# Optimization experiments

Measured on AMD Instinct MI355X. Metric: run time of the kernel, lower is better.

## Reference

```python
import jax, jax.numpy as jnp
import numpy as np

C_IN = 128
C_QK = C_IN // 8


def setup_inputs() -> dict:
    key = jax.random.key(0)
    kx, kq, kk, kv = jax.random.split(key, 4)
    x = jax.random.normal(kx, (8, C_IN, 64, 64), dtype=jnp.float32)
    # 1x1 conv weights, stored as (c_out, c_in); fan-in scaled init
    s = 1.0 / np.sqrt(C_IN)
    Wq = jax.random.normal(kq, (C_QK, C_IN), dtype=jnp.float32) * s
    Wk = jax.random.normal(kk, (C_QK, C_IN), dtype=jnp.float32) * s
    Wv = jax.random.normal(kv, (C_IN, C_IN), dtype=jnp.float32) * s
    gamma = jnp.ones((1,), dtype=jnp.float32) * 0.5  # nonzero so residual branch matters
    return {"x": x, "Wq": Wq, "Wk": Wk, "Wv": Wv, "gamma": gamma}


def reference(x, Wq, Wk, Wv, gamma):
    b, c, h, w = x.shape
    xt = rearr = x.reshape(b, c, h * w)            # b c n
    q = jnp.einsum('oc,bcn->bno', Wq, xt)          # b n c//8
    k = jnp.einsum('oc,bcn->bon', Wk, xt)          # b c//8 n
    v = jnp.einsum('oc,bcn->bno', Wv, xt)          # b n c
    energy = jnp.einsum('bno,bom->bnm', q, k)      # b n n (no scale, per source)
    attn = jax.nn.softmax(energy, axis=-1)
    out = jnp.einsum('bnm,bmc->bnc', attn, v)      # b n c
    out = out.transpose(0, 2, 1).reshape(b, c, h, w)
    return x + gamma[0] * out
```

## Files before the change

### kernel.cpp

```cpp
#include <hip/hip_runtime.h>
#include <hip/hip_bf16.h>


typedef __bf16 bf16x8 __attribute__((ext_vector_type(8)));
typedef __bf16 bf16x4 __attribute__((ext_vector_type(4)));
typedef float  f32x16 __attribute__((ext_vector_type(16)));

static constexpr int Bb = 8, Cc = 128, Nn = 4096, CQ = 16;

__device__ __forceinline__ f32x16 mfma32(bf16x8 a, bf16x8 b, f32x16 c) {
    return __builtin_amdgcn_mfma_f32_32x32x16_bf16(a, b, c, 0, 0, 0);
}
struct HL { __bf16 h, l; };
__device__ __forceinline__ HL hilo(float f) {
    HL r;
    r.h = (__bf16)f;
    r.l = (__bf16)(f - (float)r.h);
    return r;
}

__global__ __launch_bounds__(256) void qkv_kernel(
    const float* __restrict__ x, const float* __restrict__ Wq,
    const float* __restrict__ Wk, const float* __restrict__ Wv,
    float* __restrict__ qw, float* __restrict__ kw, __bf16* __restrict__ vw)
{
    const int b = blockIdx.y, n0 = blockIdx.x * 64, t = threadIdx.x;
    const int wave = t >> 6, lane = t & 63, lr = lane & 31, lq = lane >> 5;

    __shared__ __bf16 xh[64][136], xl[64][136];
    __shared__ __bf16 wqh[32][136], wql[32][136];
    __shared__ __bf16 wvh[128][136];

    {
        const int n = t & 63, cib = t >> 6;
        #pragma unroll 4
        for (int i = 0; i < 32; ++i) {
            int ci = cib + i * 4;
            float v = x[((size_t)(b * Cc + ci)) * Nn + n0 + n];
            HL z = hilo(v);
            xh[n][ci] = z.h; xl[n][ci] = z.l;
        }
    }
    #pragma unroll
    for (int i = 0; i < 8; ++i) {
        int idx = t + i * 256;
        int o = idx >> 7, ci = idx & 127;
        HL zq = hilo(Wq[idx]);
        wqh[o][ci] = zq.h; wql[o][ci] = zq.l;
        HL zk = hilo(Wk[idx]);
        wqh[16 + o][ci] = zk.h; wql[16 + o][ci] = zk.l;
    }
    #pragma unroll
    for (int i = 0; i < 16; ++i) {
        int flat = t * 4 + i * 1024;
        float4 w4 = *(const float4*)(Wv + flat);
        int c = flat >> 7, ci0 = flat & 127;
        bf16x4 h4 = { (__bf16)w4.x, (__bf16)w4.y, (__bf16)w4.z, (__bf16)w4.w };
        *(bf16x4*)&wvh[c][ci0] = h4;
    }
    __syncthreads();

    if (wave < 2) {
        const int nh = wave;
        f32x16 acc = {};
        #pragma unroll
        for (int ks = 0; ks < 8; ++ks) {
            bf16x8 ah = *(const bf16x8*)&wqh[lr][ks * 16 + lq * 8];
            bf16x8 al = *(const bf16x8*)&wql[lr][ks * 16 + lq * 8];
            bf16x8 bh = *(const bf16x8*)&xh[nh * 32 + lr][ks * 16 + lq * 8];
            bf16x8 bl = *(const bf16x8*)&xl[nh * 32 + lr][ks * 16 + lq * 8];
            acc = mfma32(ah, bh, acc);
            acc = mfma32(al, bh, acc);
            acc = mfma32(ah, bl, acc);
        }
        const int n = n0 + nh * 32 + lr;
        #pragma unroll
        for (int r = 0; r < 16; ++r) {
            int op = (r & 3) + 8 * (r >> 2) + 4 * lq;
            if (op < 16) qw[((size_t)(b * Nn + n)) * CQ + op] = acc[r];
            else         kw[((size_t)(b * Nn + n)) * CQ + (op - 16)] = acc[r];
        }
    }
    {
        int tl[3][2]; int nt;
        if      (wave == 0) { tl[0][0]=2; tl[0][1]=0; nt=1; }
        else if (wave == 1) { tl[0][0]=2; tl[0][1]=1; nt=1; }
        else if (wave == 2) { tl[0][0]=0; tl[0][1]=0; tl[1][0]=1; tl[1][1]=0; tl[2][0]=3; tl[2][1]=0; nt=3; }
        else                { tl[0][0]=0; tl[0][1]=1; tl[1][0]=1; tl[1][1]=1; tl[2][0]=3; tl[2][1]=1; nt=3; }
        for (int ti = 0; ti < nt; ++ti) {
            const int ct = tl[ti][0], nh = tl[ti][1];
            f32x16 acc = {};
            #pragma unroll
            for (int ks = 0; ks < 8; ++ks) {
                bf16x8 a  = *(const bf16x8*)&wvh[ct * 32 + lr][ks * 16 + lq * 8];
                bf16x8 bh = *(const bf16x8*)&xh[nh * 32 + lr][ks * 16 + lq * 8];
                acc = mfma32(a, bh, acc);
            }
            const int n = n0 + nh * 32 + lr;
            #pragma unroll
            for (int r = 0; r < 16; ++r) {
                int c = (r & 3) + 8 * (r >> 2) + 4 * lq + ct * 32;
                vw[((size_t)(b * Cc + c)) * Nn + n] = (__bf16)acc[r];
            }
        }
    }
}

__global__ __launch_bounds__(256) void attn_kernel(
    const float* __restrict__ x, const float* __restrict__ qw,
    const float* __restrict__ kw, const __bf16* __restrict__ vw,
    const float* __restrict__ gamma, float* __restrict__ out)
{
    const int b = blockIdx.y, n0b = blockIdx.x * 128, t = threadIdx.x;
    const int wave = t >> 6, lane = t & 63, lr = lane & 31, lq = lane >> 5;

    __shared__ __bf16 qT[128][40];
    __shared__ __bf16 kT[64][40];
    __shared__ __bf16 vT[128][72];
    __shared__ __bf16 Pl[4][32][72];

    #pragma unroll
    for (int i = 0; i < 2; ++i) {
        int idx = t + i * 256;
        int n = idx >> 2, og = idx & 3;
        float4 q4 = *(const float4*)(qw + ((size_t)(b * Nn + n0b + n)) * CQ + og * 4);
        HL z0 = hilo(q4.x), z1 = hilo(q4.y), z2 = hilo(q4.z), z3 = hilo(q4.w);
        bf16x4 h = { z0.h, z1.h, z2.h, z3.h };
        bf16x4 l = { z0.l, z1.l, z2.l, z3.l };
        *(bf16x4*)&qT[n][og * 4] = h;
        *(bf16x4*)&qT[n][16 + og * 4] = l;
    }

    const int vc = t >> 3, vs = t & 7;
    const int kr = t >> 2, kg = t & 3;
    uint4 vreg[4]; float4 kreg;

    auto load_chunk = [&](int m0) {
        #pragma unroll
        for (int i = 0; i < 4; ++i)
            vreg[i] = *(const uint4*)(vw + ((size_t)(b * Cc + vc + 32 * i)) * Nn + m0 + vs * 8);
        kreg = *(const float4*)(kw + ((size_t)(b * Nn + m0 + kr)) * CQ + kg * 4);
    };
    auto store_chunk = [&]() {
        #pragma unroll
        for (int i = 0; i < 4; ++i)
            *(uint4*)&vT[vc + 32 * i][vs * 8] = vreg[i];
        HL z0 = hilo(kreg.x), z1 = hilo(kreg.y), z2 = hilo(kreg.z), z3 = hilo(kreg.w);
        bf16x4 h = { z0.h, z1.h, z2.h, z3.h };
        bf16x4 l = { z0.l, z1.l, z2.l, z3.l };
        *(bf16x4*)&kT[kr][kg * 4] = h;
        *(bf16x4*)&kT[kr][16 + kg * 4] = l;
    };

    load_chunk(0);
    store_chunk();
    __syncthreads();

    const bf16x8 qhi = *(const bf16x8*)&qT[wave * 32 + lr][lq * 8];
    const bf16x8 qlo = *(const bf16x8*)&qT[wave * 32 + lr][16 + lq * 8];

    f32x16 acc[4] = {{}, {}, {}, {}};
    float m_run = -3e38f, l_run = 0.f;

    for (int it = 0; it < 64; ++it) {
        load_chunk((it < 63 ? it + 1 : 63) * 64);

        f32x16 s0 = {}, s1 = {};
        {
            bf16x8 kh = *(const bf16x8*)&kT[lr][lq * 8];
            bf16x8 kl = *(const bf16x8*)&kT[lr][16 + lq * 8];
            s0 = mfma32(kh, qhi, s0); s0 = mfma32(kl, qhi, s0); s0 = mfma32(kh, qlo, s0);
            kh = *(const bf16x8*)&kT[32 + lr][lq * 8];
            kl = *(const bf16x8*)&kT[32 + lr][16 + lq * 8];
            s1 = mfma32(kh, qhi, s1); s1 = mfma32(kl, qhi, s1); s1 = mfma32(kh, qlo, s1);
        }

        float cmax = -3e38f;
        #pragma unroll
        for (int r = 0; r < 16; ++r) { cmax = fmaxf(cmax, s0[r]); cmax = fmaxf(cmax, s1[r]); }
        cmax = fmaxf(cmax, __shfl_xor(cmax, 32));
        const float mnew = fmaxf(m_run, cmax);
        const float alpha = __expf(m_run - mnew);
        float p0[16], p1[16], csum = 0.f;
        #pragma unroll
        for (int r = 0; r < 16; ++r) {
            p0[r] = __expf(s0[r] - mnew); csum += p0[r];
            p1[r] = __expf(s1[r] - mnew); csum += p1[r];
        }
        csum += __shfl_xor(csum, 32);
        l_run = l_run * alpha + csum;
        m_run = mnew;
        #pragma unroll
        for (int ct = 0; ct < 4; ++ct)
            #pragma unroll
            for (int r = 0; r < 16; ++r) acc[ct][r] *= alpha;

        #pragma unroll
        for (int g = 0; g < 4; ++g) {
            bf16x4 a = { (__bf16)p0[4*g], (__bf16)p0[4*g+1], (__bf16)p0[4*g+2], (__bf16)p0[4*g+3] };
            *(bf16x4*)&Pl[wave][lr][lq * 4 + g * 8] = a;
            bf16x4 c4 = { (__bf16)p1[4*g], (__bf16)p1[4*g+1], (__bf16)p1[4*g+2], (__bf16)p1[4*g+3] };
            *(bf16x4*)&Pl[wave][lr][32 + lq * 4 + g * 8] = c4;
        }

        bf16x8 pf[4];
        #pragma unroll
        for (int ks = 0; ks < 4; ++ks)
            pf[ks] = *(const bf16x8*)&Pl[wave][lr][ks * 16 + lq * 8];
        #pragma unroll
        for (int ct = 0; ct < 4; ++ct) {
            #pragma unroll
            for (int ks = 0; ks < 4; ++ks) {
                bf16x8 va = *(const bf16x8*)&vT[ct * 32 + lr][ks * 16 + lq * 8];
                acc[ct] = mfma32(va, pf[ks], acc[ct]);
            }
        }

        __syncthreads();
        store_chunk();
        __syncthreads();
    }

    const float g = gamma[0];
    const float linv = 1.0f / l_run;
    const int n = n0b + wave * 32 + lr;
    #pragma unroll
    for (int ct = 0; ct < 4; ++ct) {
        #pragma unroll
        for (int r = 0; r < 16; ++r) {
            int c = (r & 3) + 8 * (r >> 2) + 4 * lq + ct * 32;
            size_t idx = ((size_t)(b * Cc + c)) * Nn + n;
            out[idx] = x[idx] + g * acc[ct][r] * linv;
        }
    }
}

extern "C" void kernel_launch(void* const* d_in, const int* in_sizes, int n_in,
                              void* d_out, int out_size, void* d_ws, size_t ws_size,
                              hipStream_t stream) {
    const float* x  = (const float*)d_in[0];
    const float* Wq = (const float*)d_in[1];
    const float* Wk = (const float*)d_in[2];
    const float* Wv = (const float*)d_in[3];
    const float* gm = (const float*)d_in[4];

    float* qw = (float*)d_ws;
    float* kw = qw + (size_t)Bb * Nn * CQ;
    __bf16* vw = (__bf16*)(kw + (size_t)Bb * Nn * CQ);

    qkv_kernel<<<dim3(Nn / 64, Bb), 256, 0, stream>>>(x, Wq, Wk, Wv, qw, kw, vw);
    attn_kernel<<<dim3(Nn / 128, Bb), 256, 0, stream>>>(x, qw, kw, vw, gm,
                                                        (float*)d_out);
}
```

Before: 224.4 us.

## Split attention keys across two wave groups with double-buffered V and register P

The attention kernel now uses 512 threads, and two groups of four waves each process half of the key sequence for the same 128 queries. At the end the groups merge their softmax states and accumulators through shared memory. V tiles are double-buffered so there is one barrier per iteration instead of two. K is loaded straight into registers instead of staged through LDS, and the P matrix is rearranged with cross-lane shuffles rather than an LDS round trip. This should give more waves per CU and less synchronisation and LDS traffic, at the cost of redundant K global loads per wave, more registers, and a final merge step.

```diff
diff --git a/kernel.cpp b/kernel.cpp
--- a/kernel.cpp
+++ b/kernel.cpp
@@ -5,6 +5,8 @@
 typedef __bf16 bf16x8 __attribute__((ext_vector_type(8)));
 typedef __bf16 bf16x4 __attribute__((ext_vector_type(4)));
 typedef float  f32x16 __attribute__((ext_vector_type(16)));
+typedef unsigned int u32;
+typedef u32 u32x4 __attribute__((ext_vector_type(4)));
 
 static constexpr int Bb = 8, Cc = 128, Nn = 4096, CQ = 16;
 
@@ -17,6 +19,11 @@
     r.h = (__bf16)f;
     r.l = (__bf16)(f - (float)r.h);
     return r;
+}
+__device__ __forceinline__ u32 pack2(float a, float b) {
+    unsigned short ua = __builtin_bit_cast(unsigned short, (__bf16)a);
+    unsigned short ub = __builtin_bit_cast(unsigned short, (__bf16)b);
+    return (u32)ua | ((u32)ub << 16);
 }
 
 __global__ __launch_bounds__(256) void qkv_kernel(
@@ -106,74 +113,70 @@
     }
 }
 
-__global__ __launch_bounds__(256) void attn_kernel(
+__global__ __launch_bounds__(512) void attn_kernel(
     const float* __restrict__ x, const float* __restrict__ qw,
     const float* __restrict__ kw, const __bf16* __restrict__ vw,
     const float* __restrict__ gamma, float* __restrict__ out)
 {
     const int b = blockIdx.y, n0b = blockIdx.x * 128, t = threadIdx.x;
     const int wave = t >> 6, lane = t & 63, lr = lane & 31, lq = lane >> 5;
-
-    __shared__ __bf16 qT[128][40];
-    __shared__ __bf16 kT[64][40];
-    __shared__ __bf16 vT[128][72];
-    __shared__ __bf16 Pl[4][32][72];
-
-    #pragma unroll
-    for (int i = 0; i < 2; ++i) {
-        int idx = t + i * 256;
-        int n = idx >> 2, og = idx & 3;
-        float4 q4 = *(const float4*)(qw + ((size_t)(b * Nn + n0b + n)) * CQ + og * 4);
-        HL z0 = hilo(q4.x), z1 = hilo(q4.y), z2 = hilo(q4.z), z3 = hilo(q4.w);
-        bf16x4 h = { z0.h, z1.h, z2.h, z3.h };
-        bf16x4 l = { z0.l, z1.l, z2.l, z3.l };
-        *(bf16x4*)&qT[n][og * 4] = h;
-        *(bf16x4*)&qT[n][16 + og * 4] = l;
-    }
-
-    const int vc = t >> 3, vs = t & 7;
-    const int kr = t >> 2, kg = t & 3;
-    uint4 vreg[4]; float4 kreg;
-
-    auto load_chunk = [&](int m0) {
-        #pragma unroll
-        for (int i = 0; i < 4; ++i)
-            vreg[i] = *(const uint4*)(vw + ((size_t)(b * Cc + vc + 32 * i)) * Nn + m0 + vs * 8);
-        kreg = *(const float4*)(kw + ((size_t)(b * Nn + m0 + kr)) * CQ + kg * 4);
+    const int qg = wave & 3, half = wave >> 2;
+    const int kbase = half * 2048;
+
+    __shared__ __bf16 vT[2][2][128][72];
+
+    const int u = t & 255;
+    const int sc = u >> 1, sm = (u & 1) * 32;
+
+    auto loadV = [&](int chunk, uint4* r) {
+        const __bf16* base = vw + ((size_t)(b * Cc + sc)) * Nn + kbase + chunk * 64 + sm;
+        #pragma unroll
+        for (int i = 0; i < 4; ++i) r[i] = *(const uint4*)(base + 8 * i);
     };
-    auto store_chunk = [&]() {
-        #pragma unroll
-        for (int i = 0; i < 4; ++i)
-            *(uint4*)&vT[vc + 32 * i][vs * 8] = vreg[i];
-        HL z0 = hilo(kreg.x), z1 = hilo(kreg.y), z2 = hilo(kreg.z), z3 = hilo(kreg.w);
-        bf16x4 h = { z0.h, z1.h, z2.h, z3.h };
-        bf16x4 l = { z0.l, z1.l, z2.l, z3.l };
-        *(bf16x4*)&kT[kr][kg * 4] = h;
-        *(bf16x4*)&kT[kr][16 + kg * 4] = l;
+    auto storeV = [&](int buf, const uint4* r) {
+        #pragma unroll
+        for (int i = 0; i < 4; ++i) *(uint4*)&vT[half][buf][sc][sm + 8 * i] = r[i];
     };
 
-    load_chunk(0);
-    store_chunk();
+    const int nq = n0b + qg * 32 + lr;
+    bf16x8 qhi, qlo;
+    {
+        float qa[8];
+        *(float4*)&qa[0] = *(const float4*)(qw + ((size_t)b * Nn + nq) * CQ + lq * 8);
+        *(float4*)&qa[4] = *(const float4*)(qw + ((size_t)b * Nn + nq) * CQ + lq * 8 + 4);
+        #pragma unroll
+        for (int j = 0; j < 8; ++j) { HL z = hilo(qa[j]); qhi[j] = z.h; qlo[j] = z.l; }
+    }
+
+    uint4 vr[4];
+    loadV(0, vr); storeV(0, vr);
+    loadV(1, vr);
     __syncthreads();
-
-    const bf16x8 qhi = *(const bf16x8*)&qT[wave * 32 + lr][lq * 8];
-    const bf16x8 qlo = *(const bf16x8*)&qT[wave * 32 + lr][16 + lq * 8];
 
     f32x16 acc[4] = {{}, {}, {}, {}};
     float m_run = -3e38f, l_run = 0.f;
 
-    for (int it = 0; it < 64; ++it) {
-        load_chunk((it < 63 ? it + 1 : 63) * 64);
+    for (int it = 0; it < 32; ++it) {
+        const int p = it & 1;
+
+        const size_t krow = (size_t)b * Nn + kbase + it * 64;
+        bf16x8 k0h, k0l, k1h, k1l;
+        {
+            float ka[8], kb[8];
+            *(float4*)&ka[0] = *(const float4*)(kw + (krow + lr) * CQ + lq * 8);
+            *(float4*)&ka[4] = *(const float4*)(kw + (krow + lr) * CQ + lq * 8 + 4);
+            *(float4*)&kb[0] = *(const float4*)(kw + (krow + 32 + lr) * CQ + lq * 8);
+            *(float4*)&kb[4] = *(const float4*)(kw + (krow + 32 + lr) * CQ + lq * 8 + 4);
+            #pragma unroll
+            for (int j = 0; j < 8; ++j) {
+                HL z = hilo(ka[j]); k0h[j] = z.h; k0l[j] = z.l;
+                HL w = hilo(kb[j]); k1h[j] = w.h; k1l[j] = w.l;
+            }
+        }
 
         f32x16 s0 = {}, s1 = {};
-        {
-            bf16x8 kh = *(const bf16x8*)&kT[lr][lq * 8];
-            bf16x8 kl = *(const bf16x8*)&kT[lr][16 + lq * 8];
-            s0 = mfma32(kh, qhi, s0); s0 = mfma32(kl, qhi, s0); s0 = mfma32(kh, qlo, s0);
-            kh = *(const bf16x8*)&kT[32 + lr][lq * 8];
-            kl = *(const bf16x8*)&kT[32 + lr][16 + lq * 8];
-            s1 = mfma32(kh, qhi, s1); s1 = mfma32(kl, qhi, s1); s1 = mfma32(kh, qlo, s1);
-        }
+        s0 = mfma32(k0h, qhi, s0); s0 = mfma32(k0l, qhi, s0); s0 = mfma32(k0h, qlo, s0);
+        s1 = mfma32(k1h, qhi, s1); s1 = mfma32(k1l, qhi, s1); s1 = mfma32(k1h, qlo, s1);
 
         float cmax = -3e38f;
         #pragma unroll
@@ -195,43 +198,70 @@
             #pragma unroll
             for (int r = 0; r < 16; ++r) acc[ct][r] *= alpha;
 
+        u32 Qk[16], Sh[16];
         #pragma unroll
         for (int g = 0; g < 4; ++g) {
-            bf16x4 a = { (__bf16)p0[4*g], (__bf16)p0[4*g+1], (__bf16)p0[4*g+2], (__bf16)p0[4*g+3] };
-            *(bf16x4*)&Pl[wave][lr][lq * 4 + g * 8] = a;
-            bf16x4 c4 = { (__bf16)p1[4*g], (__bf16)p1[4*g+1], (__bf16)p1[4*g+2], (__bf16)p1[4*g+3] };
-            *(bf16x4*)&Pl[wave][lr][32 + lq * 4 + g * 8] = c4;
-        }
+            Qk[g * 2]     = pack2(p0[4 * g],     p0[4 * g + 1]);
+            Qk[g * 2 + 1] = pack2(p0[4 * g + 2], p0[4 * g + 3]);
+            Qk[8 + g * 2]     = pack2(p1[4 * g],     p1[4 * g + 1]);
+            Qk[8 + g * 2 + 1] = pack2(p1[4 * g + 2], p1[4 * g + 3]);
+        }
+        #pragma unroll
+        for (int i = 0; i < 16; ++i) Sh[i] = (u32)__shfl_xor((int)Qk[i], 32);
 
         bf16x8 pf[4];
         #pragma unroll
-        for (int ks = 0; ks < 4; ++ks)
-            pf[ks] = *(const bf16x8*)&Pl[wave][lr][ks * 16 + lq * 8];
+        for (int ks = 0; ks < 4; ++ks) {
+            int z = 2 * ks + lq, base = (z >> 2) * 8 + (z & 3) * 2;
+            u32x4 w;
+            if (lq == 0) { w[0] = Qk[base]; w[1] = Qk[base + 1]; w[2] = Sh[base]; w[3] = Sh[base + 1]; }
+            else         { w[0] = Sh[base]; w[1] = Sh[base + 1]; w[2] = Qk[base]; w[3] = Qk[base + 1]; }
+            pf[ks] = __builtin_bit_cast(bf16x8, w);
+        }
+
         #pragma unroll
         for (int ct = 0; ct < 4; ++ct) {
             #pragma unroll
             for (int ks = 0; ks < 4; ++ks) {
-                bf16x8 va = *(const bf16x8*)&vT[ct * 32 + lr][ks * 16 + lq * 8];
+                bf16x8 va = *(const bf16x8*)&vT[half][p][ct * 32 + lr][ks * 16 + lq * 8];
                 acc[ct] = mfma32(va, pf[ks], acc[ct]);
             }
         }
 
+        storeV(1 - p, vr);
+        if (it + 2 < 32) loadV(it + 2, vr);
         __syncthreads();
-        store_chunk();
-        __syncthreads();
-    }
-
-    const float g = gamma[0];
-    const float linv = 1.0f / l_run;
-    const int n = n0b + wave * 32 + lr;
-    #pragma unroll
-    for (int ct = 0; ct < 4; ++ct) {
-        #pragma unroll
-        for (int r = 0; r < 16; ++r) {
-            int c = (r & 3) + 8 * (r >> 2) + 4 * lq + ct * 32;
-            size_t idx = ((size_t)(b * Cc + c)) * Nn + n;
-            out[idx] = x[idx] + g * acc[ct][r] * linv;
-        }
+    }
+
+    float* mrg = (float*)&vT[0][0][0][0];
+    float* Og  = mrg + qg * (32 * 129);
+    float* ml  = mrg + 4 * (32 * 129) + qg * 64;
+
+    if (half == 1) {
+        if (lq == 0) { ml[lr] = m_run; ml[32 + lr] = l_run; }
+        #pragma unroll
+        for (int ct = 0; ct < 4; ++ct)
+            #pragma unroll
+            for (int r = 0; r < 16; ++r) {
+                int c = (r & 3) + 8 * (r >> 2) + 4 * lq + 32 * ct;
+                Og[lr * 129 + c] = acc[ct][r];
+            }
+    }
+    __syncthreads();
+    if (half == 0) {
+        const float m2 = ml[lr], l2 = ml[32 + lr];
+        const float mm = fmaxf(m_run, m2);
+        const float e1 = __expf(m_run - mm), e2 = __expf(m2 - mm);
+        const float linv = 1.0f / (e1 * l_run + e2 * l2);
+        const float gg = gamma[0];
+        #pragma unroll
+        for (int ct = 0; ct < 4; ++ct)
+            #pragma unroll
+            for (int r = 0; r < 16; ++r) {
+                int c = (r & 3) + 8 * (r >> 2) + 4 * lq + 32 * ct;
+                size_t idx = ((size_t)(b * Cc + c)) * Nn + nq;
+                out[idx] = x[idx] + gg * (e1 * acc[ct][r] + e2 * Og[lr * 129 + c]) * linv;
+            }
     }
 }
 
@@ -249,6 +279,6 @@
     __bf16* vw = (__bf16*)(kw + (size_t)Bb * Nn * CQ);
 
     qkv_kernel<<<dim3(Nn / 64, Bb), 256, 0, stream>>>(x, Wq, Wk, Wv, qw, kw, vw);
-    attn_kernel<<<dim3(Nn / 128, Bb), 256, 0, stream>>>(x, qw, kw, vw, gm,
+    attn_kernel<<<dim3(Nn / 128, Bb), 512, 0, stream>>>(x, qw, kw, vw, gm,
                                                         (float*)d_out);
 }
```

Result: slower. 239.4 us (+6.7%).
